# Optimization experiments

Measured on AMD Instinct MI355X. Metric: run time of the kernel, lower is better.

Reference implementation:

```python
import jax, jax.numpy as jnp
import numpy as np

N_CH = 256          # EEG channels = graph nodes
T = 100000          # timesteps
CNN_OUT = 32
GRU_H = 64
GNN_H = 32
N_CLS = 2
THRESH = 0.7


def _conv1d(x, w, b, stride, pad):
    # x: [N, C_in, L], w: [C_out, C_in, K]
    y = jax.lax.conv_general_dilated(
        x, w, window_strides=(stride,), padding=[(pad, pad)],
        dimension_numbers=("NCH", "OIH", "NCH"))
    return y + b[None, :, None]


def _gru_last_hidden(xs, wih, whh, bih, bhh):
    # xs: [S, N, in], returns final hidden [N, H] (PyTorch GRU equations)
    H = whh.shape[1]
    h0 = jnp.zeros((xs.shape[1], H), xs.dtype)

    def step(h, x):
        gi = x @ wih.T + bih          # [N, 3H]
        gh = h @ whh.T + bhh
        i_r, i_z, i_n = jnp.split(gi, 3, axis=-1)
        h_r, h_z, h_n = jnp.split(gh, 3, axis=-1)
        r = jax.nn.sigmoid(i_r + h_r)
        z = jax.nn.sigmoid(i_z + h_z)
        n = jnp.tanh(i_n + r * h_n)
        h = (1.0 - z) * n + z * h
        return h, None

    hT, _ = jax.lax.scan(step, h0, xs)
    return hT


def _pairwise_corrcoef(x):
    x = x - x.mean(axis=1, keepdims=True)
    x = x / (x.std(axis=1, keepdims=True, ddof=1) + 1e-6)  # torch std is unbiased
    return (x @ x.T) / x.shape[1]


def _gcn(x, A_hat, w, b):
    # PyG GCNConv: A_hat @ (x @ W^T) + b  (sym-normalized adj w/ self-loops)
    return A_hat @ (x @ w.T) + b


def setup_inputs() -> dict:
    key = jax.random.key(0)
    ks = jax.random.split(key, 24)
    r = lambda i, shape, s: (jax.random.normal(ks[i], shape, jnp.float32) * s)
    d = {
        "data": r(0, (N_CH, T), 1.0),
        "conv1_w": r(1, (8, 1, 11), 0.3), "conv1_b": r(2, (8,), 0.1),
        "conv2_w": r(3, (16, 8, 7), 0.1), "conv2_b": r(4, (16,), 0.1),
        "conv3_w": r(5, (CNN_OUT, 16, 5), 0.1), "conv3_b": r(6, (CNN_OUT,), 0.1),
        "gru_wih_f": r(7, (3 * GRU_H, CNN_OUT), 0.1), "gru_whh_f": r(8, (3 * GRU_H, GRU_H), 0.1),
        "gru_bih_f": r(9, (3 * GRU_H,), 0.05), "gru_bhh_f": r(10, (3 * GRU_H,), 0.05),
        "gru_wih_b": r(11, (3 * GRU_H, CNN_OUT), 0.1), "gru_whh_b": r(12, (3 * GRU_H, GRU_H), 0.1),
        "gru_bih_b": r(13, (3 * GRU_H,), 0.05), "gru_bhh_b": r(14, (3 * GRU_H,), 0.05),
        "gcn1_w": r(15, (GNN_H, 2 * GRU_H), 0.1), "gcn1_b": r(16, (GNN_H,), 0.05),
        "gcn2_w": r(17, (GNN_H, GNN_H), 0.15), "gcn2_b": r(18, (GNN_H,), 0.05),
        "cls_w": r(19, (N_CLS, GNN_H), 0.15), "cls_b": r(20, (N_CLS,), 0.05),
    }
    return d


def reference(data, conv1_w, conv1_b, conv2_w, conv2_b, conv3_w, conv3_b,
              gru_wih_f, gru_whh_f, gru_bih_f, gru_bhh_f,
              gru_wih_b, gru_whh_b, gru_bih_b, gru_bhh_b,
              gcn1_w, gcn1_b, gcn2_w, gcn2_b, cls_w, cls_b):
    x = data[:, None, :]                                 # [N, 1, T]
    x = jax.nn.relu(_conv1d(x, conv1_w, conv1_b, 5, 5))  # [N, 8, 20000]
    x = jax.nn.relu(_conv1d(x, conv2_w, conv2_b, 5, 3))  # [N, 16, 4000]
    x = jax.nn.relu(_conv1d(x, conv3_w, conv3_b, 5, 2))  # [N, 32, 800]
    xs = jnp.transpose(x, (2, 0, 1))                     # [S=800, N, 32]

    h_f = _gru_last_hidden(xs, gru_wih_f, gru_whh_f, gru_bih_f, gru_bhh_f)
    h_b = _gru_last_hidden(xs[::-1], gru_wih_b, gru_whh_b, gru_bih_b, gru_bhh_b)
    # torch h_n.permute(1,0,2).reshape(N,-1) -> concat [fwd, bwd]
    h_n = jnp.concatenate([h_f, h_b], axis=-1)           # [N, 128]

    corr = _pairwise_corrcoef(h_n)                       # [N, N]
    # dense adjacency = thresholded |corr|; diagonal is ~1 so self-loops present
    # (matches PyG add_remaining_self_loops: already there). Always nonempty.
    A = (jnp.abs(corr) > THRESH).astype(h_n.dtype)
    deg = A.sum(axis=1)
    dinv = jax.lax.rsqrt(jnp.maximum(deg, 1e-12))
    A_hat = A * dinv[:, None] * dinv[None, :]            # D^-1/2 A D^-1/2

    h = jax.nn.relu(_gcn(h_n, A_hat, gcn1_w, gcn1_b))
    h = jax.nn.relu(_gcn(h, A_hat, gcn2_w, gcn2_b))
    graph_emb = h.mean(axis=0, keepdims=True)            # [1, GNN_H]
    return graph_emb @ cls_w.T + cls_b                   # [1, N_CLS]
```

## Files before the change

kernel.cpp:

```cpp
#include <hip/hip_runtime.h>
#include <math.h>

#define N_CH 256
#define T_IN 100000
#define L1O 20000
#define L2O 4000
#define L3O 800
#define C1 8
#define C2 16
#define C3 32

#define TILE3 25
#define NY2   125
#define NY1   627
#define ND    3141

#define KEEP1(x) asm volatile("" : "+v"(x))

__device__ __forceinline__ float sigm(float x) {
    x = fminf(fmaxf(x, -30.0f), 30.0f);
    return 1.0f / (1.0f + __expf(-x));
}
__device__ __forceinline__ float tanhfast(float x) {
    x = fminf(fmaxf(x, -15.0f), 15.0f);
    float e = __expf(-2.0f * x);
    return (1.0f - e) / (1.0f + e);
}
__device__ __forceinline__ float dot4(float4 a, float4 b) {
    return a.x * b.x + a.y * b.y + a.z * b.z + a.w * b.w;
}
__device__ __forceinline__ float bcast(float v, int lane) {
    return __int_as_float(__builtin_amdgcn_readlane(__float_as_int(v), lane));
}

__global__ __launch_bounds__(256) void k_conv(
    const float* __restrict__ data,
    const float* __restrict__ w1, const float* __restrict__ b1,
    const float* __restrict__ w2, const float* __restrict__ b2,
    const float* __restrict__ w3, const float* __restrict__ b3,
    float* __restrict__ x3)
{
    __shared__ __align__(16) float sd[ND];
    __shared__ __align__(16) float sy1[NY1][C1];
    __shared__ __align__(16) float sy2[NY2][C2];
    __shared__ __align__(16) float sw1[C1 * 11];
    __shared__ float sb1[C1];
    __shared__ __align__(16) float sw2[C2 * C1 * 7];
    __shared__ float sb2[C2];
    __shared__ __align__(16) float sw3[C3 * C2 * 5];
    __shared__ float sb3[C3];

    const int tid = threadIdx.x;
    const int tb  = blockIdx.x;
    const int ch  = blockIdx.y;
    const int t0    = tb * TILE3;
    const int dbase = 3125 * tb - 70;
    const int ubase = 625 * tb - 13;
    const int sbase = 125 * tb - 2;

    for (int e = tid; e < C1 * 11;    e += 256) sw1[e] = w1[e];
    for (int e = tid; e < C1;         e += 256) sb1[e] = b1[e];
    for (int e = tid; e < C2 * C1 * 7; e += 256) sw2[e] = w2[e];
    for (int e = tid; e < C2;         e += 256) sb2[e] = b2[e];
    for (int e = tid; e < C3 * C2 * 5; e += 256) sw3[e] = w3[e];
    for (int e = tid; e < C3;         e += 256) sb3[e] = b3[e];

    const float* dch = data + (size_t)ch * T_IN;
    for (int e = tid; e < ND; e += 256) {
        int g = dbase + e;
        sd[e] = (g >= 0 && g < T_IN) ? dch[g] : 0.0f;
    }
    __syncthreads();

    {
        const int c = tid & 7;
        float wr[11];
        #pragma unroll
        for (int k = 0; k < 11; ++k) wr[k] = sw1[c * 11 + k];
        const float bb = sb1[c];
        for (int u = tid >> 3; u < NY1; u += 32) {
            int ug = ubase + u;
            float acc = bb;
            #pragma unroll
            for (int k = 0; k < 11; ++k) acc += wr[k] * sd[5 * u + k];
            sy1[u][c] = (ug >= 0 && ug < L1O) ? fmaxf(acc, 0.0f) : 0.0f;
        }
    }
    __syncthreads();

    {
        const int c = tid & 15;
        float wr[56];
        #pragma unroll
        for (int q = 0; q < 14; ++q)
            ((float4*)wr)[q] = ((const float4*)(sw2 + c * 56))[q];
        const float bb = sb2[c];
        for (int s = tid >> 4; s < NY2; s += 16) {
            int sg = sbase + s;
            float acc = bb;
            #pragma unroll
            for (int k = 0; k < 7; ++k) {
                const float4* y4 = (const float4*)&sy1[5 * s + k][0];
                float4 ya = y4[0], yb = y4[1];
                acc += wr[0*7+k]*ya.x + wr[1*7+k]*ya.y + wr[2*7+k]*ya.z + wr[3*7+k]*ya.w
                     + wr[4*7+k]*yb.x + wr[5*7+k]*yb.y + wr[6*7+k]*yb.z + wr[7*7+k]*yb.w;
            }
            sy2[s][c] = (sg >= 0 && sg < L2O) ? fmaxf(acc, 0.0f) : 0.0f;
        }
    }
    __syncthreads();

    {
        const int o = tid & 31;
        float wr[80];
        #pragma unroll
        for (int q = 0; q < 20; ++q)
            ((float4*)wr)[q] = ((const float4*)(sw3 + o * 80))[q];
        const float bb = sb3[o];
        for (int tl = tid >> 5; tl < TILE3; tl += 8) {
            float acc = bb;
            #pragma unroll
            for (int k = 0; k < 5; ++k) {
                const float4* y4 = (const float4*)&sy2[5 * tl + k][0];
                float4 za = y4[0], zb = y4[1], zc = y4[2], zd = y4[3];
                acc += wr[0*5+k]*za.x  + wr[1*5+k]*za.y  + wr[2*5+k]*za.z  + wr[3*5+k]*za.w
                     + wr[4*5+k]*zb.x  + wr[5*5+k]*zb.y  + wr[6*5+k]*zb.z  + wr[7*5+k]*zb.w
                     + wr[8*5+k]*zc.x  + wr[9*5+k]*zc.y  + wr[10*5+k]*zc.z + wr[11*5+k]*zc.w
                     + wr[12*5+k]*zd.x + wr[13*5+k]*zd.y + wr[14*5+k]*zd.z + wr[15*5+k]*zd.w;
            }
            x3[((size_t)ch * L3O + (t0 + tl)) * C3 + o] = fmaxf(acc, 0.0f);
        }
    }
}

__global__ __launch_bounds__(192) void k_gi(
    const float* __restrict__ x3,
    const float* __restrict__ wih_f, const float* __restrict__ bih_f,
    const float* __restrict__ wih_b, const float* __restrict__ bih_b,
    float* __restrict__ Gi, int c0, int CH)
{
    const int row = threadIdx.x;
    const int dirch = blockIdx.x;
    const int dir = dirch >> 8, ch = dirch & 255;
    const int tt0 = blockIdx.y * 25;
    const float* wih = dir ? wih_b : wih_f;
    const float* bih = dir ? bih_b : bih_f;
    __shared__ __align__(16) float sx[25][32];

    for (int e = row; e < 25 * 32; e += 192) {
        int tt = e >> 5, k = e & 31;
        int step = c0 + tt0 + tt;
        int tm = dir ? (L3O - 1 - step) : step;
        sx[tt][k] = x3[((size_t)ch * L3O + tm) * 32 + k];
    }
    float4 w[8];
    const float4* w4 = (const float4*)(wih + row * 32);
    #pragma unroll
    for (int q = 0; q < 8; ++q) w[q] = w4[q];
    const float bb = bih[row];
    __syncthreads();

    float* gout = Gi + ((size_t)dirch * CH + tt0) * 192 + row;
    for (int tt = 0; tt < 25; ++tt) {
        const float4* x4 = (const float4*)&sx[tt][0];
        float a0 = 0, a1 = 0, a2 = 0, a3 = 0;
        #pragma unroll
        for (int q = 0; q < 8; q += 4) {
            a0 += dot4(w[q],     x4[q]);
            a1 += dot4(w[q + 1], x4[q + 1]);
            a2 += dot4(w[q + 2], x4[q + 2]);
            a3 += dot4(w[q + 3], x4[q + 3]);
        }
        gout[tt * 192] = bb + ((a0 + a1) + (a2 + a3));
    }
}

__global__ __launch_bounds__(64, 1) void k_gru3(
    const float* __restrict__ Gi,
    const float* __restrict__ whh_f, const float* __restrict__ bhh_f,
    const float* __restrict__ whh_b, const float* __restrict__ bhh_b,
    float* __restrict__ hN, int t0, int tlen, int CH)
{
    const int lane = threadIdx.x;
    const int ch = blockIdx.x, dir = blockIdx.y;
    const int dirch = dir * 256 + ch;
    const float* whh = dir ? whh_b : whh_f;
    const float* bhh = dir ? bhh_b : bhh_f;

    float wr[64], wz[64], wn[64];
    const float4* whh4 = (const float4*)whh;
    #pragma unroll
    for (int q = 0; q < 16; ++q) {
        float4 a = whh4[(0   + lane) * 16 + q];
        float4 b = whh4[(64  + lane) * 16 + q];
        float4 c = whh4[(128 + lane) * 16 + q];
        wr[4*q] = a.x; wr[4*q+1] = a.y; wr[4*q+2] = a.z; wr[4*q+3] = a.w;
        wz[4*q] = b.x; wz[4*q+1] = b.y; wz[4*q+2] = b.z; wz[4*q+3] = b.w;
        wn[4*q] = c.x; wn[4*q+1] = c.y; wn[4*q+2] = c.z; wn[4*q+3] = c.w;
    }
    #pragma unroll
    for (int j = 0; j < 64; ++j) { KEEP1(wr[j]); KEEP1(wz[j]); KEEP1(wn[j]); }

    const float bhr = bhh[lane], bhz = bhh[64 + lane], bhn = bhh[128 + lane];

    float h = (t0 == 0) ? 0.0f : hN[ch * 128 + dir * 64 + lane];

    const float* gp = Gi + (size_t)dirch * CH * 192;
    float g0r = gp[lane], g0z = gp[64 + lane], g0n = gp[128 + lane];
    gp += 192;
    float g1r = gp[lane], g1z = gp[64 + lane], g1n = gp[128 + lane];
    gp += 192;

    for (int tl = 0; tl < tlen; ++tl) {
        float g2r = 0.f, g2z = 0.f, g2n = 0.f;
        if (tl + 2 < tlen) { g2r = gp[lane]; g2z = gp[64 + lane]; g2n = gp[128 + lane]; }
        gp += 192;

        float ar0 = 0.f, ar1 = 0.f, az0 = 0.f, az1 = 0.f, an0 = 0.f, an1 = 0.f;
        #pragma unroll
        for (int j = 0; j < 64; j += 2) {
            float hj0 = bcast(h, j);
            float hj1 = bcast(h, j + 1);
            ar0 = fmaf(wr[j],     hj0, ar0);
            az0 = fmaf(wz[j],     hj0, az0);
            an0 = fmaf(wn[j],     hj0, an0);
            ar1 = fmaf(wr[j + 1], hj1, ar1);
            az1 = fmaf(wz[j + 1], hj1, az1);
            an1 = fmaf(wn[j + 1], hj1, an1);
        }
        float r = sigm(g0r + bhr + (ar0 + ar1));
        float z = sigm(g0z + bhz + (az0 + az1));
        float n = tanhfast(g0n + r * ((an0 + an1) + bhn));
        h = (1.0f - z) * n + z * h;

        g0r = g1r; g0z = g1z; g0n = g1n;
        g1r = g2r; g1z = g2z; g1n = g2n;
    }
    hN[ch * 128 + dir * 64 + lane] = h;
}

#define CHUNK 100
__global__ __launch_bounds__(64) void k_gru(
    const float* __restrict__ x3,
    const float* __restrict__ wih_f, const float* __restrict__ whh_f,
    const float* __restrict__ bih_f, const float* __restrict__ bhh_f,
    const float* __restrict__ wih_b, const float* __restrict__ whh_b,
    const float* __restrict__ bih_b, const float* __restrict__ bhh_b,
    float* __restrict__ hN)
{
    const int lane = threadIdx.x;
    const int ch   = blockIdx.x;
    const int dir  = blockIdx.y;
    const float* wih = dir ? wih_b : wih_f;
    const float* whh = dir ? whh_b : whh_f;
    const float* bih = dir ? bih_b : bih_f;
    const float* bhh = dir ? bhh_b : bhh_f;

    __shared__ __align__(16) float sh[64];
    __shared__ __align__(16) float sx[CHUNK * 32];

    float4 wir[8], wiz[8], win[8];
    const float4* wih4 = (const float4*)wih;
    #pragma unroll
    for (int k = 0; k < 8; ++k) {
        wir[k] = wih4[(0   + lane) * 8 + k];
        wiz[k] = wih4[(64  + lane) * 8 + k];
        win[k] = wih4[(128 + lane) * 8 + k];
    }
    float4 whr[16], whz[16], whn[16];
    const float4* whh4 = (const float4*)whh;
    #pragma unroll
    for (int j = 0; j < 16; ++j) {
        whr[j] = whh4[(0   + lane) * 16 + j];
        whz[j] = whh4[(64  + lane) * 16 + j];
        whn[j] = whh4[(128 + lane) * 16 + j];
    }
    const float bir = bih[lane], biz = bih[64 + lane], bin_ = bih[128 + lane];
    const float bhr = bhh[lane], bhz = bhh[64 + lane], bhn  = bhh[128 + lane];

    float h = 0.0f;
    sh[lane] = 0.0f;
    __syncthreads();

    const float* xch = x3 + (size_t)ch * L3O * 32;
    for (int c0 = 0; c0 < L3O; c0 += CHUNK) {
        for (int e = lane; e < CHUNK * 32; e += 64) {
            int tt = e >> 5, k = e & 31;
            int sidx = c0 + tt;
            int t = dir ? (L3O - 1 - sidx) : sidx;
            sx[e] = xch[t * 32 + k];
        }
        __syncthreads();
        for (int tl = 0; tl < CHUNK; ++tl) {
            const float4* xv4 = (const float4*)(sx + tl * 32);
            float gr = 0.f, gz = 0.f, gn = 0.f;
            #pragma unroll
            for (int k = 0; k < 8; ++k) {
                float4 x4 = xv4[k];
                gr += dot4(wir[k], x4); gz += dot4(wiz[k], x4); gn += dot4(win[k], x4);
            }
            float hr = 0.f, hz = 0.f, hn = 0.f;
            const float4* sh4 = (const float4*)sh;
            #pragma unroll
            for (int j = 0; j < 16; ++j) {
                float4 h4 = sh4[j];
                hr += dot4(whr[j], h4); hz += dot4(whz[j], h4); hn += dot4(whn[j], h4);
            }
            float r = sigm(gr + bir + hr + bhr);
            float z = sigm(gz + biz + hz + bhz);
            float n = tanhfast(gn + bin_ + r * (hn + bhn));
            h = (1.0f - z) * n + z * h;
            __syncthreads();
            sh[lane] = h;
            __syncthreads();
        }
    }
    hN[ch * 128 + dir * 64 + lane] = h;
}

__global__ __launch_bounds__(128) void k_norm(
    const float* __restrict__ hN, const float* __restrict__ gcn1_w,
    float* __restrict__ Xn, float* __restrict__ XnT, float* __restrict__ hw1)
{
    const int i = blockIdx.x, tid = threadIdx.x;
    __shared__ float red[128];
    __shared__ float row[128];
    float v = hN[i * 128 + tid];
    row[tid] = v;
    red[tid] = v;
    __syncthreads();
    for (int s = 64; s > 0; s >>= 1) { if (tid < s) red[tid] += red[tid + s]; __syncthreads(); }
    float mean = red[0] / 128.0f;
    __syncthreads();
    float d = v - mean;
    red[tid] = d * d;
    __syncthreads();
    for (int s = 64; s > 0; s >>= 1) { if (tid < s) red[tid] += red[tid + s]; __syncthreads(); }
    float sd = sqrtf(red[0] / 127.0f);
    float xn = d / (sd + 1e-6f);
    Xn[i * 128 + tid] = xn;
    XnT[tid * 256 + i] = xn;
    if (tid < 32) {
        float acc = 0.f;
        for (int k = 0; k < 128; ++k) acc += row[k] * gcn1_w[tid * 128 + k];
        hw1[i * 32 + tid] = acc;
    }
}

__global__ __launch_bounds__(256) void k_corr(
    const float* __restrict__ Xn, const float* __restrict__ XnT,
    float* __restrict__ A, float* __restrict__ deg)
{
    const int i = blockIdx.x, tid = threadIdx.x;
    __shared__ float xi[128];
    __shared__ float red[256];
    if (tid < 128) xi[tid] = Xn[i * 128 + tid];
    __syncthreads();
    float c = 0.f;
    for (int k = 0; k < 128; ++k) c += xi[k] * XnT[k * 256 + tid];
    c *= (1.0f / 128.0f);
    float a = (fabsf(c) > 0.7f) ? 1.0f : 0.0f;
    A[i * 256 + tid] = a;
    red[tid] = a;
    __syncthreads();
    for (int s = 128; s > 0; s >>= 1) { if (tid < s) red[tid] += red[tid + s]; __syncthreads(); }
    if (tid == 0) deg[i] = red[0];
}

__global__ __launch_bounds__(256) void k_gcn(
    const float* __restrict__ A, const float* __restrict__ deg,
    const float* __restrict__ hw, const float* __restrict__ bias,
    const float* __restrict__ wNext,
    float* __restrict__ hOut, float* __restrict__ hwNext)
{
    const int i = blockIdx.x, tid = threadIdx.x;
    const int f = tid & 31, grp = tid >> 5;
    __shared__ float aj[256];
    __shared__ float red[8][32];
    __shared__ float hrow[32];
    float dj = rsqrtf(fmaxf(deg[tid], 1e-12f));
    aj[tid] = A[i * 256 + tid] * dj;
    __syncthreads();
    float p = 0.f;
    for (int j = grp * 32; j < grp * 32 + 32; ++j) p += aj[j] * hw[j * 32 + f];
    red[grp][f] = p;
    __syncthreads();
    if (grp == 0) {
        float s = 0.f;
        #pragma unroll
        for (int g = 0; g < 8; ++g) s += red[g][f];
        float di = rsqrtf(fmaxf(deg[i], 1e-12f));
        float o = fmaxf(bias[f] + di * s, 0.0f);
        hOut[i * 32 + f] = o;
        hrow[f] = o;
    }
    __syncthreads();
    if (wNext != nullptr && grp == 0) {
        float acc = 0.f;
        #pragma unroll
        for (int k = 0; k < 32; ++k) acc += hrow[k] * wNext[f * 32 + k];
        hwNext[i * 32 + f] = acc;
    }
}

__global__ __launch_bounds__(64) void k_head(
    const float* __restrict__ h2, const float* __restrict__ cls_w,
    const float* __restrict__ cls_b, float* __restrict__ out)
{
    const int tid = threadIdx.x;
    __shared__ float mean[32];
    if (tid < 32) {
        float s = 0.f;
        for (int i = 0; i < 256; ++i) s += h2[i * 32 + tid];
        mean[tid] = s * (1.0f / 256.0f);
    }
    __syncthreads();
    if (tid < 2) {
        float s = cls_b[tid];
        #pragma unroll
        for (int fe = 0; fe < 32; ++fe) s += mean[fe] * cls_w[tid * 32 + fe];
        out[tid] = s;
    }
}

extern "C" void kernel_launch(void* const* d_in, const int* in_sizes, int n_in,
                              void* d_out, int out_size, void* d_ws, size_t ws_size,
                              hipStream_t stream) {
    const float* data    = (const float*)d_in[0];
    const float* conv1_w = (const float*)d_in[1];
    const float* conv1_b = (const float*)d_in[2];
    const float* conv2_w = (const float*)d_in[3];
    const float* conv2_b = (const float*)d_in[4];
    const float* conv3_w = (const float*)d_in[5];
    const float* conv3_b = (const float*)d_in[6];
    const float* wih_f   = (const float*)d_in[7];
    const float* whh_f   = (const float*)d_in[8];
    const float* bih_f   = (const float*)d_in[9];
    const float* bhh_f   = (const float*)d_in[10];
    const float* wih_b   = (const float*)d_in[11];
    const float* whh_b   = (const float*)d_in[12];
    const float* bih_b   = (const float*)d_in[13];
    const float* bhh_b   = (const float*)d_in[14];
    const float* gcn1_w  = (const float*)d_in[15];
    const float* gcn1_b  = (const float*)d_in[16];
    const float* gcn2_w  = (const float*)d_in[17];
    const float* gcn2_b  = (const float*)d_in[18];
    const float* cls_w   = (const float*)d_in[19];
    const float* cls_b   = (const float*)d_in[20];

    float* ws  = (float*)d_ws;
    float* x3  = ws;
    float* hN  = x3 + 6553600;
    float* Xn  = hN + 32768;
    float* XnT = Xn + 32768;
    float* A   = XnT + 32768;
    float* deg = A + 65536;
    float* hw1 = deg + 256;
    float* h1  = hw1 + 8192;
    float* hw2 = h1 + 8192;
    float* h2  = hw2 + 8192;
    float* Gi  = h2 + 8192;

    const size_t BASE = 6726272;
    const size_t avail = ws_size / 4;
    int CH = 0;
    if      (avail >= BASE + (size_t)512 * 800 * 192) CH = 800;
    else if (avail >= BASE + (size_t)512 * 100 * 192) CH = 100;
    else if (avail >= BASE + (size_t)512 *  50 * 192) CH = 50;
    else if (avail >= BASE + (size_t)512 *  25 * 192) CH = 25;

    k_conv<<<dim3(32, 256), 256, 0, stream>>>(data, conv1_w, conv1_b, conv2_w, conv2_b,
                                              conv3_w, conv3_b, x3);
    if (CH) {
        for (int c0 = 0; c0 < L3O; c0 += CH) {
            k_gi<<<dim3(512, CH / 25), 192, 0, stream>>>(x3, wih_f, bih_f, wih_b, bih_b,
                                                         Gi, c0, CH);
            k_gru3<<<dim3(256, 2), 64, 0, stream>>>(Gi, whh_f, bhh_f, whh_b, bhh_b,
                                                    hN, c0, CH, CH);
        }
    } else {
        k_gru<<<dim3(256, 2), 64, 0, stream>>>(x3, wih_f, whh_f, bih_f, bhh_f,
                                               wih_b, whh_b, bih_b, bhh_b, hN);
    }
    k_norm<<<256, 128, 0, stream>>>(hN, gcn1_w, Xn, XnT, hw1);
    k_corr<<<256, 256, 0, stream>>>(Xn, XnT, A, deg);
    k_gcn<<<256, 256, 0, stream>>>(A, deg, hw1, gcn1_b, gcn2_w, h1, hw2);
    k_gcn<<<256, 256, 0, stream>>>(A, deg, hw2, gcn2_b, nullptr, h2, nullptr);
    k_head<<<1, 64, 0, stream>>>(h2, cls_w, cls_b, (float*)d_out);
}
```

Measured before the change: 977.7 us.

## Fuse GRU input projection into recurrence with gate-split 3-wave blocks

Replaces the separate input-projection kernel plus per-step recurrence kernel (and the Gi workspace buffer) with one fused kernel. Each block now uses three wavefronts, one per gate row group, each holding its own 64 recurrent and 32 input weights in registers. The input projection is computed per step through cross-lane broadcasts of the prefetched x values. Gate partial sums are exchanged through double-buffered shared memory with one barrier per step. This removes the Gi global round-trip and the many chunked launches, at the cost of a block-wide sync in every serial step and extra per-step input-projection work on the critical path.

```diff
diff --git a/kernel.cpp b/kernel.cpp
--- a/kernel.cpp
+++ b/kernel.cpp
@@ -133,189 +133,105 @@
     }
 }
 
-__global__ __launch_bounds__(192) void k_gi(
+__global__ __launch_bounds__(192, 1) void k_gru4(
     const float* __restrict__ x3,
     const float* __restrict__ wih_f, const float* __restrict__ bih_f,
+    const float* __restrict__ whh_f, const float* __restrict__ bhh_f,
     const float* __restrict__ wih_b, const float* __restrict__ bih_b,
-    float* __restrict__ Gi, int c0, int CH)
-{
-    const int row = threadIdx.x;
-    const int dirch = blockIdx.x;
-    const int dir = dirch >> 8, ch = dirch & 255;
-    const int tt0 = blockIdx.y * 25;
-    const float* wih = dir ? wih_b : wih_f;
-    const float* bih = dir ? bih_b : bih_f;
-    __shared__ __align__(16) float sx[25][32];
-
-    for (int e = row; e < 25 * 32; e += 192) {
-        int tt = e >> 5, k = e & 31;
-        int step = c0 + tt0 + tt;
-        int tm = dir ? (L3O - 1 - step) : step;
-        sx[tt][k] = x3[((size_t)ch * L3O + tm) * 32 + k];
-    }
-    float4 w[8];
-    const float4* w4 = (const float4*)(wih + row * 32);
-    #pragma unroll
-    for (int q = 0; q < 8; ++q) w[q] = w4[q];
-    const float bb = bih[row];
-    __syncthreads();
-
-    float* gout = Gi + ((size_t)dirch * CH + tt0) * 192 + row;
-    for (int tt = 0; tt < 25; ++tt) {
-        const float4* x4 = (const float4*)&sx[tt][0];
-        float a0 = 0, a1 = 0, a2 = 0, a3 = 0;
-        #pragma unroll
-        for (int q = 0; q < 8; q += 4) {
-            a0 += dot4(w[q],     x4[q]);
-            a1 += dot4(w[q + 1], x4[q + 1]);
-            a2 += dot4(w[q + 2], x4[q + 2]);
-            a3 += dot4(w[q + 3], x4[q + 3]);
-        }
-        gout[tt * 192] = bb + ((a0 + a1) + (a2 + a3));
-    }
-}
-
-__global__ __launch_bounds__(64, 1) void k_gru3(
-    const float* __restrict__ Gi,
-    const float* __restrict__ whh_f, const float* __restrict__ bhh_f,
     const float* __restrict__ whh_b, const float* __restrict__ bhh_b,
-    float* __restrict__ hN, int t0, int tlen, int CH)
-{
-    const int lane = threadIdx.x;
+    float* __restrict__ hN)
+{
+    const int tid  = threadIdx.x;
+    const int lane = tid & 63;
+    const int g    = tid >> 6;
     const int ch = blockIdx.x, dir = blockIdx.y;
-    const int dirch = dir * 256 + ch;
-    const float* whh = dir ? whh_b : whh_f;
-    const float* bhh = dir ? bhh_b : bhh_f;
-
-    float wr[64], wz[64], wn[64];
-    const float4* whh4 = (const float4*)whh;
-    #pragma unroll
-    for (int q = 0; q < 16; ++q) {
-        float4 a = whh4[(0   + lane) * 16 + q];
-        float4 b = whh4[(64  + lane) * 16 + q];
-        float4 c = whh4[(128 + lane) * 16 + q];
-        wr[4*q] = a.x; wr[4*q+1] = a.y; wr[4*q+2] = a.z; wr[4*q+3] = a.w;
-        wz[4*q] = b.x; wz[4*q+1] = b.y; wz[4*q+2] = b.z; wz[4*q+3] = b.w;
-        wn[4*q] = c.x; wn[4*q+1] = c.y; wn[4*q+2] = c.z; wn[4*q+3] = c.w;
-    }
-    #pragma unroll
-    for (int j = 0; j < 64; ++j) { KEEP1(wr[j]); KEEP1(wz[j]); KEEP1(wn[j]); }
-
-    const float bhr = bhh[lane], bhz = bhh[64 + lane], bhn = bhh[128 + lane];
-
-    float h = (t0 == 0) ? 0.0f : hN[ch * 128 + dir * 64 + lane];
-
-    const float* gp = Gi + (size_t)dirch * CH * 192;
-    float g0r = gp[lane], g0z = gp[64 + lane], g0n = gp[128 + lane];
-    gp += 192;
-    float g1r = gp[lane], g1z = gp[64 + lane], g1n = gp[128 + lane];
-    gp += 192;
-
-    for (int tl = 0; tl < tlen; ++tl) {
-        float g2r = 0.f, g2z = 0.f, g2n = 0.f;
-        if (tl + 2 < tlen) { g2r = gp[lane]; g2z = gp[64 + lane]; g2n = gp[128 + lane]; }
-        gp += 192;
-
-        float ar0 = 0.f, ar1 = 0.f, az0 = 0.f, az1 = 0.f, an0 = 0.f, an1 = 0.f;
-        #pragma unroll
-        for (int j = 0; j < 64; j += 2) {
-            float hj0 = bcast(h, j);
-            float hj1 = bcast(h, j + 1);
-            ar0 = fmaf(wr[j],     hj0, ar0);
-            az0 = fmaf(wz[j],     hj0, az0);
-            an0 = fmaf(wn[j],     hj0, an0);
-            ar1 = fmaf(wr[j + 1], hj1, ar1);
-            az1 = fmaf(wz[j + 1], hj1, az1);
-            an1 = fmaf(wn[j + 1], hj1, an1);
-        }
-        float r = sigm(g0r + bhr + (ar0 + ar1));
-        float z = sigm(g0z + bhz + (az0 + az1));
-        float n = tanhfast(g0n + r * ((an0 + an1) + bhn));
-        h = (1.0f - z) * n + z * h;
-
-        g0r = g1r; g0z = g1z; g0n = g1n;
-        g1r = g2r; g1z = g2z; g1n = g2n;
-    }
-    hN[ch * 128 + dir * 64 + lane] = h;
-}
-
-#define CHUNK 100
-__global__ __launch_bounds__(64) void k_gru(
-    const float* __restrict__ x3,
-    const float* __restrict__ wih_f, const float* __restrict__ whh_f,
-    const float* __restrict__ bih_f, const float* __restrict__ bhh_f,
-    const float* __restrict__ wih_b, const float* __restrict__ whh_b,
-    const float* __restrict__ bih_b, const float* __restrict__ bhh_b,
-    float* __restrict__ hN)
-{
-    const int lane = threadIdx.x;
-    const int ch   = blockIdx.x;
-    const int dir  = blockIdx.y;
     const float* wih = dir ? wih_b : wih_f;
     const float* whh = dir ? whh_b : whh_f;
     const float* bih = dir ? bih_b : bih_f;
     const float* bhh = dir ? bhh_b : bhh_f;
-
-    __shared__ __align__(16) float sh[64];
-    __shared__ __align__(16) float sx[CHUNK * 32];
-
-    float4 wir[8], wiz[8], win[8];
-    const float4* wih4 = (const float4*)wih;
+    const int row = g * 64 + lane;
+
+    __shared__ float sdot[2][4][64];
+
+    float w[64];
+    {
+        const float4* w4 = (const float4*)(whh + row * 64);
+        #pragma unroll
+        for (int q = 0; q < 16; ++q) {
+            float4 v = w4[q];
+            w[4*q] = v.x; w[4*q+1] = v.y; w[4*q+2] = v.z; w[4*q+3] = v.w;
+        }
+    }
+    float wi[32];
+    {
+        const float4* w4 = (const float4*)(wih + row * 32);
+        #pragma unroll
+        for (int q = 0; q < 8; ++q) {
+            float4 v = w4[q];
+            wi[4*q] = v.x; wi[4*q+1] = v.y; wi[4*q+2] = v.z; wi[4*q+3] = v.w;
+        }
+    }
     #pragma unroll
-    for (int k = 0; k < 8; ++k) {
-        wir[k] = wih4[(0   + lane) * 8 + k];
-        wiz[k] = wih4[(64  + lane) * 8 + k];
-        win[k] = wih4[(128 + lane) * 8 + k];
-    }
-    float4 whr[16], whz[16], whn[16];
-    const float4* whh4 = (const float4*)whh;
+    for (int j = 0; j < 64; ++j) KEEP1(w[j]);
     #pragma unroll
-    for (int j = 0; j < 16; ++j) {
-        whr[j] = whh4[(0   + lane) * 16 + j];
-        whz[j] = whh4[(64  + lane) * 16 + j];
-        whn[j] = whh4[(128 + lane) * 16 + j];
-    }
-    const float bir = bih[lane], biz = bih[64 + lane], bin_ = bih[128 + lane];
-    const float bhr = bhh[lane], bhz = bhh[64 + lane], bhn  = bhh[128 + lane];
+    for (int j = 0; j < 32; ++j) KEEP1(wi[j]);
+
+    const float bi = bih[row];
+    const float bh = bhh[row];
+
+    const float* xp = x3 + (size_t)ch * L3O * 32 + (lane & 31);
+    const int xstride = dir ? -32 : 32;
+    if (dir) xp += (size_t)(L3O - 1) * 32;
+
+    float x0 = xp[0]; xp += xstride;
+    float x1 = xp[0]; xp += xstride;
+    float x2 = xp[0]; xp += xstride;
 
     float h = 0.0f;
-    sh[lane] = 0.0f;
-    __syncthreads();
-
-    const float* xch = x3 + (size_t)ch * L3O * 32;
-    for (int c0 = 0; c0 < L3O; c0 += CHUNK) {
-        for (int e = lane; e < CHUNK * 32; e += 64) {
-            int tt = e >> 5, k = e & 31;
-            int sidx = c0 + tt;
-            int t = dir ? (L3O - 1 - sidx) : sidx;
-            sx[e] = xch[t * 32 + k];
+
+    for (int s = 0; s < L3O; ++s) {
+        float xnext = 0.0f;
+        if (s + 3 < L3O) xnext = xp[0];
+        xp += xstride;
+
+        float a0 = bi, a0b = 0.0f;
+        #pragma unroll
+        for (int k = 0; k < 32; k += 2) {
+            a0  = fmaf(wi[k],     bcast(x0, k),     a0);
+            a0b = fmaf(wi[k + 1], bcast(x0, k + 1), a0b);
+        }
+        float a1 = bh, a1b = 0.0f, a1c = 0.0f, a1d = 0.0f;
+        #pragma unroll
+        for (int j = 0; j < 64; j += 4) {
+            a1  = fmaf(w[j],     bcast(h, j),     a1);
+            a1b = fmaf(w[j + 1], bcast(h, j + 1), a1b);
+            a1c = fmaf(w[j + 2], bcast(h, j + 2), a1c);
+            a1d = fmaf(w[j + 3], bcast(h, j + 3), a1d);
+        }
+        float ai = a0 + a0b;
+        float ah = (a1 + a1b) + (a1c + a1d);
+
+        const int p = s & 1;
+        if (g < 2) {
+            sdot[p][g][lane] = ai + ah;
+        } else {
+            sdot[p][2][lane] = ah;
+            sdot[p][3][lane] = ai;
         }
         __syncthreads();
-        for (int tl = 0; tl < CHUNK; ++tl) {
-            const float4* xv4 = (const float4*)(sx + tl * 32);
-            float gr = 0.f, gz = 0.f, gn = 0.f;
-            #pragma unroll
-            for (int k = 0; k < 8; ++k) {
-                float4 x4 = xv4[k];
-                gr += dot4(wir[k], x4); gz += dot4(wiz[k], x4); gn += dot4(win[k], x4);
-            }
-            float hr = 0.f, hz = 0.f, hn = 0.f;
-            const float4* sh4 = (const float4*)sh;
-            #pragma unroll
-            for (int j = 0; j < 16; ++j) {
-                float4 h4 = sh4[j];
-                hr += dot4(whr[j], h4); hz += dot4(whz[j], h4); hn += dot4(whn[j], h4);
-            }
-            float r = sigm(gr + bir + hr + bhr);
-            float z = sigm(gz + biz + hz + bhz);
-            float n = tanhfast(gn + bin_ + r * (hn + bhn));
-            h = (1.0f - z) * n + z * h;
-            __syncthreads();
-            sh[lane] = h;
-            __syncthreads();
-        }
-    }
-    hN[ch * 128 + dir * 64 + lane] = h;
+
+        float sr  = sdot[p][0][lane];
+        float sz  = sdot[p][1][lane];
+        float shn = sdot[p][2][lane];
+        float sin_= sdot[p][3][lane];
+        float r = sigm(sr);
+        float z = sigm(sz);
+        float n = tanhfast(sin_ + r * shn);
+        h = (1.0f - z) * n + z * h;
+
+        x0 = x1; x1 = x2; x2 = xnext;
+    }
+    if (g == 0) hN[ch * 128 + dir * 64 + lane] = h;
 }
 
 __global__ __launch_bounds__(128) void k_norm(
@@ -459,29 +375,11 @@
     float* h1  = hw1 + 8192;
     float* hw2 = h1 + 8192;
     float* h2  = hw2 + 8192;
-    float* Gi  = h2 + 8192;
-
-    const size_t BASE = 6726272;
-    const size_t avail = ws_size / 4;
-    int CH = 0;
-    if      (avail >= BASE + (size_t)512 * 800 * 192) CH = 800;
-    else if (avail >= BASE + (size_t)512 * 100 * 192) CH = 100;
-    else if (avail >= BASE + (size_t)512 *  50 * 192) CH = 50;
-    else if (avail >= BASE + (size_t)512 *  25 * 192) CH = 25;
 
     k_conv<<<dim3(32, 256), 256, 0, stream>>>(data, conv1_w, conv1_b, conv2_w, conv2_b,
                                               conv3_w, conv3_b, x3);
-    if (CH) {
-        for (int c0 = 0; c0 < L3O; c0 += CH) {
-            k_gi<<<dim3(512, CH / 25), 192, 0, stream>>>(x3, wih_f, bih_f, wih_b, bih_b,
-                                                         Gi, c0, CH);
-            k_gru3<<<dim3(256, 2), 64, 0, stream>>>(Gi, whh_f, bhh_f, whh_b, bhh_b,
-                                                    hN, c0, CH, CH);
-        }
-    } else {
-        k_gru<<<dim3(256, 2), 64, 0, stream>>>(x3, wih_f, whh_f, bih_f, bhh_f,
-                                               wih_b, whh_b, bih_b, bhh_b, hN);
-    }
+    k_gru4<<<dim3(256, 2), 192, 0, stream>>>(x3, wih_f, bih_f, whh_f, bhh_f,
+                                             wih_b, bih_b, whh_b, bhh_b, hN);
     k_norm<<<256, 128, 0, stream>>>(hN, gcn1_w, Xn, XnT, hw1);
     k_corr<<<256, 256, 0, stream>>>(Xn, XnT, A, deg);
     k_gcn<<<256, 256, 0, stream>>>(A, deg, hw1, gcn1_b, gcn2_w, h1, hw2);
```

Result: slower. 1.195 ms (+22.2%).
